# Kernel optimization log

Measured on AMD Instinct MI355X. Metric: run time of the kernel, lower is better.

## Reference

```python
import jax, jax.numpy as jnp
import numpy as np

B, N, C = 4, 4096, 1024
H, M = 16, 64          # num_heads, num_landmarks
DH = C // H
SCALE = H ** (-0.5)    # faithful to source: num_heads**-0.5
LN_EPS = 1e-5


def setup_inputs() -> dict:
    key = jax.random.key(0)
    ks = jax.random.split(key, 8)
    s = 0.02
    return {
        "x": jax.random.normal(ks[0], (B, N, C), jnp.float32),
        "ln_w": jnp.ones((C,), jnp.float32),
        "ln_b": jnp.zeros((C,), jnp.float32),
        "qkv_w": jax.random.normal(ks[1], (3 * C, C), jnp.float32) * s,
        "qkv_b": jax.random.normal(ks[2], (3 * C,), jnp.float32) * s,
        "gamma_w": jax.random.normal(ks[3], (C, C), jnp.float32) * s,
        "gamma_b": jax.random.normal(ks[4], (C,), jnp.float32) * s,
        "proj_w": jax.random.normal(ks[5], (C, C), jnp.float32) * s,
        "proj_b": jax.random.normal(ks[6], (C,), jnp.float32) * s,
    }


def _iterative_inv(K, n_iter=6):
    # Newton-Schulz pseudo-inverse on [..., M, M]
    Id = jnp.eye(K.shape[-1], dtype=K.dtype)
    KA = jnp.abs(K)
    V0 = KA.sum(axis=-2, keepdims=True).max(axis=-1, keepdims=True)
    VI = KA.sum(axis=-1, keepdims=True).max(axis=-2, keepdims=True)
    V = jnp.swapaxes(K, -2, -1) / (V0 * VI)
    for _ in range(n_iter):
        KV = K @ V
        V = 0.25 * V @ (13.0 * Id - KV @ (15.0 * Id - KV @ (7.0 * Id - KV)))
    return V


def reference(x, ln_w, ln_b, qkv_w, qkv_b, gamma_w, gamma_b, proj_w, proj_b):
    # LayerNorm
    mu = x.mean(axis=-1, keepdims=True)
    var = x.var(axis=-1, keepdims=True)
    xn = (x - mu) * jax.lax.rsqrt(var + LN_EPS) * ln_w + ln_b
    # qkv: (B,N,3C) -> (3,B,H,N,DH)
    qkv = (xn @ qkv_w.T + qkv_b).reshape(B, N, 3, H, DH).transpose(2, 0, 3, 1, 4)
    q, k, v = qkv[0], qkv[1], qkv[2]
    # landmarks: mean-pool segments of length N//M, then scale
    q_lm = q.reshape(B, H, M, N // M, DH).mean(axis=-2) * SCALE  # (B,H,M,DH)
    k_lm = k.reshape(B, H, M, N // M, DH).mean(axis=-2) * SCALE
    attn1 = jax.nn.softmax(jnp.einsum('bhnd,bhmd->bhnm', q, k_lm), axis=-1)    # (B,H,N,M)
    attn2 = jax.nn.softmax(jnp.einsum('bhmd,bhld->bhml', q_lm, k_lm), axis=-1)  # (B,H,M,M)
    attn3 = jax.nn.softmax(jnp.einsum('bhmd,bhnd->bhmn', q_lm, k), axis=-1)    # (B,H,M,N)
    attn2_inv = _iterative_inv(attn2)
    out = attn1 @ (attn2_inv @ (attn3 @ v))            # (B,H,N,DH)
    out = out.transpose(0, 2, 1, 3).reshape(B, N, C)
    out = out @ gamma_w.T + gamma_b                    # LipNorm=True branch
    out = out @ proj_w.T + proj_b                      # proj (dropout p=0 is identity)
    return out
```

## Files before the change

kernel.cpp:

```cpp
#include <hip/hip_runtime.h>
#include <stdint.h>

typedef unsigned short u16;
typedef short bf16x8 __attribute__((ext_vector_type(8)));
typedef float f32x4 __attribute__((ext_vector_type(4)));

#define MFMA16(a, b, c) __builtin_amdgcn_mfma_f32_16x16x32_bf16((a), (b), (c), 0, 0, 0)

static __device__ __forceinline__ float bfu2f(u16 u) {
  union { unsigned int i; float f; } z; z.i = ((unsigned int)u) << 16; return z.f;
}
static __device__ __forceinline__ u16 f2bfu(float f) {
  union { float f; unsigned int i; } z; z.f = f;
  unsigned int i = z.i;
  return (u16)((i + 0x7fffu + ((i >> 16) & 1u)) >> 16);
}

__device__ __forceinline__ void gload_lds16(const void* g, void* l) {
  __builtin_amdgcn_global_load_lds((const __attribute__((address_space(1))) void*)g,
                                   (__attribute__((address_space(3))) void*)l, 16, 0, 0);
}

__global__ __launch_bounds__(256) void ln_kernel(
    const float* __restrict__ x, const float* __restrict__ w,
    const float* __restrict__ b, u16* __restrict__ xn) {
  int row = blockIdx.x;
  int t = threadIdx.x;
  const float4* xr = (const float4*)(x + (size_t)row * 1024);
  float4 v = xr[t];
  float s = v.x + v.y + v.z + v.w;
  float ss = v.x * v.x + v.y * v.y + v.z * v.z + v.w * v.w;
#pragma unroll
  for (int m = 1; m < 64; m <<= 1) { s += __shfl_xor(s, m); ss += __shfl_xor(ss, m); }
  __shared__ float sb[4], ssb[4];
  int lane = t & 63, wvi = t >> 6;
  if (lane == 0) { sb[wvi] = s; ssb[wvi] = ss; }
  __syncthreads();
  s = sb[0] + sb[1] + sb[2] + sb[3];
  ss = ssb[0] + ssb[1] + ssb[2] + ssb[3];
  float mu = s * (1.0f / 1024.0f);
  float var = ss * (1.0f / 1024.0f) - mu * mu;
  float rstd = rsqrtf(var + 1e-5f);
  float4 wv4 = ((const float4*)w)[t];
  float4 bv4 = ((const float4*)b)[t];
  ushort4 o;
  o.x = f2bfu((v.x - mu) * rstd * wv4.x + bv4.x);
  o.y = f2bfu((v.y - mu) * rstd * wv4.y + bv4.y);
  o.z = f2bfu((v.z - mu) * rstd * wv4.z + bv4.z);
  o.w = f2bfu((v.w - mu) * rstd * wv4.w + bv4.w);
  ((ushort4*)xn)[(size_t)row * 256 + t] = o;
}

__global__ void cvt3_kernel(const float* __restrict__ a, u16* __restrict__ oa, int na,
                            const float* __restrict__ b, u16* __restrict__ ob, int nb,
                            const float* __restrict__ c, u16* __restrict__ oc, int nc) {
  int total = (na + nb + nc) >> 2;
  for (int i = blockIdx.x * blockDim.x + threadIdx.x; i < total; i += gridDim.x * blockDim.x) {
    int j = i << 2;
    const float* s; u16* d; int off;
    if (j < na) { s = a; d = oa; off = j; }
    else if (j < na + nb) { s = b; d = ob; off = j - na; }
    else { s = c; d = oc; off = j - na - nb; }
    float4 v = *(const float4*)(s + off);
    ushort4 o;
    o.x = f2bfu(v.x); o.y = f2bfu(v.y); o.z = f2bfu(v.z); o.w = f2bfu(v.w);
    *(ushort4*)(d + off) = o;
  }
}

template <int MODE>
__global__ __launch_bounds__(512, 2) void gemm_bt(
    const u16* __restrict__ A, const u16* __restrict__ Bw,
    const float* __restrict__ bias,
    float* __restrict__ Cf, u16* __restrict__ Cb,
    u16* __restrict__ Qo, u16* __restrict__ Ko, u16* __restrict__ Vo,
    int M, int N, int K) {
  __shared__ __attribute__((aligned(16))) u16 As[2][16384];
  __shared__ __attribute__((aligned(16))) u16 Bs[2][16384];
  int tid = threadIdx.x;
  int lane = tid & 63;
  int w = tid >> 6;
  int wr = w >> 2, wc = w & 3;
  int r16 = lane & 15, hi = lane >> 4;
  int l8 = lane >> 3, li = lane & 7;
  int bx = blockIdx.x, by = blockIdx.y;

  const char* Abase = (const char*)(A + (size_t)by * 256 * K);
  const char* Bbase = (const char*)(Bw + (size_t)bx * 256 * K);
  size_t rowbytes = (size_t)K * 2;
  int colsw = (li ^ l8) << 4;
  int nkt = K >> 6;

  f32x4 z4 = {0.f, 0.f, 0.f, 0.f};
  f32x4 acc[8][4];
#pragma unroll
  for (int m = 0; m < 8; ++m)
#pragma unroll
    for (int n = 0; n < 4; ++n) acc[m][n] = z4;

#define SG_A(buf, t, r0)                                                      \
  gload_lds16(Abase + (size_t)((r0) + w * 8 + l8) * rowbytes + ((t) << 7) +   \
                  colsw,                                                      \
              (char*)As[buf] + ((r0) + w * 8) * 128)
#define SG_B(buf, t, r0)                                                      \
  gload_lds16(Bbase + (size_t)((r0) + w * 8 + l8) * rowbytes + ((t) << 7) +   \
                  colsw,                                                      \
              (char*)Bs[buf] + ((r0) + w * 8) * 128)

  SG_A(0, 0, 0); SG_A(0, 0, 64); SG_A(0, 0, 128); SG_A(0, 0, 192);
  SG_B(0, 0, 0); SG_B(0, 0, 64); SG_B(0, 0, 128); SG_B(0, 0, 192);
  SG_A(1, 1, 0); SG_A(1, 1, 128); SG_B(1, 1, 0); SG_B(1, 1, 64);
  SG_A(1, 1, 64); SG_A(1, 1, 192);
  asm volatile("s_waitcnt vmcnt(6)" ::: "memory");
  __builtin_amdgcn_s_barrier();
  __builtin_amdgcn_sched_barrier(0);

  int buf = 0;
  bf16x8 af[4][2], bfr[4][2];

#define LDA(mh)                                                               \
  _Pragma("unroll") for (int m = 0; m < 4; ++m) {                             \
    int row = wr * 128 + (mh) * 64 + m * 16 + r16;                            \
    int sw = (row & 7) << 4;                                                  \
    _Pragma("unroll") for (int kk = 0; kk < 2; ++kk)                          \
        af[m][kk] = *(const bf16x8*)(ab + row * 128 +                         \
                                     (((kk << 6) | (hi << 4)) ^ sw));         \
  }
#define LDB(nh)                                                               \
  _Pragma("unroll") for (int n = 0; n < 2; ++n) {                             \
    int row = wc * 64 + (nh) * 32 + n * 16 + r16;                             \
    int sw = (row & 7) << 4;                                                  \
    _Pragma("unroll") for (int kk = 0; kk < 2; ++kk)                          \
        bfr[(nh) * 2 + n][kk] = *(const bf16x8*)(ab2 + row * 128 +            \
                                     (((kk << 6) | (hi << 4)) ^ sw));         \
  }
#define MM(mh, nh)                                                            \
  __builtin_amdgcn_s_setprio(1);                                              \
  _Pragma("unroll") for (int kk = 0; kk < 2; ++kk)                            \
      _Pragma("unroll") for (int m = 0; m < 4; ++m)                           \
          _Pragma("unroll") for (int n = 0; n < 2; ++n)                       \
              acc[(mh) * 4 + m][(nh) * 2 + n] =                               \
      MFMA16(af[m][kk], bfr[(nh) * 2 + n][kk], acc[(mh) * 4 + m][(nh) * 2 + n]); \
  __builtin_amdgcn_s_setprio(0)

#define BAR1                                                                  \
  __builtin_amdgcn_s_barrier();                                               \
  __builtin_amdgcn_sched_barrier(0)
#define BAR2                                                                  \
  __builtin_amdgcn_sched_barrier(0);                                          \
  __builtin_amdgcn_s_barrier();                                               \
  __builtin_amdgcn_sched_barrier(0)

  for (int t = 0; t < nkt; ++t) {
    const char* ab = (const char*)As[buf];
    const char* ab2 = (const char*)Bs[buf];
    bool s1 = (t + 1 < nkt), s2 = (t + 2 < nkt);
    LDA(0);
    LDB(0);
    if (s1) { SG_B(buf ^ 1, t + 1, 128); SG_B(buf ^ 1, t + 1, 192); }
    BAR1;
    MM(0, 0);
    BAR2;
    LDB(1);
    if (s2) { SG_A(buf, t + 2, 0); SG_A(buf, t + 2, 128); }
    BAR1;
    MM(0, 1);
    BAR2;
    LDA(1);
    if (s2) { SG_B(buf, t + 2, 0); SG_B(buf, t + 2, 64); }
    BAR1;
    MM(1, 0);
    BAR2;
    if (s2) { SG_A(buf, t + 2, 64); SG_A(buf, t + 2, 192); }
    BAR1;
    MM(1, 1);
    __builtin_amdgcn_sched_barrier(0);
    if (s2) {
      asm volatile("s_waitcnt vmcnt(6)" ::: "memory");
    } else {
      asm volatile("s_waitcnt vmcnt(0)" ::: "memory");
    }
    __builtin_amdgcn_s_barrier();
    __builtin_amdgcn_sched_barrier(0);
    buf ^= 1;
  }
#undef SG_A
#undef SG_B
#undef LDA
#undef LDB
#undef MM
#undef BAR1
#undef BAR2

#pragma unroll
  for (int m = 0; m < 8; ++m)
#pragma unroll
    for (int n = 0; n < 4; ++n)
#pragma unroll
      for (int r = 0; r < 4; ++r) {
        int row = by * 256 + wr * 128 + m * 16 + hi * 4 + r;
        int col = bx * 256 + wc * 64 + n * 16 + r16;
        float val = acc[m][n][r] + bias[col];
        if (MODE == 0) {
          Cb[(size_t)row * N + col] = f2bfu(val);
        } else if (MODE == 1) {
          Cf[(size_t)row * N + col] = val;
        } else {
          int bb = row >> 12, nt = row & 4095;
          int jt = col >> 10, h = (col >> 6) & 15, dh = col & 63;
          u16* dst = (jt == 0) ? Qo : (jt == 1) ? Ko : Vo;
          dst[(((size_t)bb * 16 + h) * 4096 + nt) * 64 + dh] = f2bfu(val);
        }
      }
}

__global__ __launch_bounds__(64) void landmark_kernel(
    const u16* __restrict__ Q, const u16* __restrict__ K,
    float* __restrict__ qlmf, u16* __restrict__ qlmb,
    float* __restrict__ klmf, u16* __restrict__ klmb) {
  int bm = blockIdx.x;
  int bh = bm >> 6, m = bm & 63;
  int d = threadIdx.x;
  const u16* src = blockIdx.y ? K : Q;
  const u16* p = src + (((size_t)bh * 4096) + m * 64) * 64 + d;
  float s = 0.f;
#pragma unroll 8
  for (int r = 0; r < 64; ++r) s += bfu2f(p[(size_t)r * 64]);
  float val = s * (0.25f / 64.0f);
  size_t o = (size_t)bh * 4096 + m * 64 + d;
  if (blockIdx.y) { klmf[o] = val; klmb[o] = f2bfu(val); }
  else            { qlmf[o] = val; qlmb[o] = f2bfu(val); }
}

__global__ __launch_bounds__(256) void attn3_pv_kernel(
    const u16* __restrict__ qlmb, const u16* __restrict__ Kmat,
    const u16* __restrict__ Vmat, float* __restrict__ Upart,
    float* __restrict__ rspart) {
  __shared__ __attribute__((aligned(16))) u16 Elds[4][8192];
  int chunk = blockIdx.x, bh = blockIdx.y;
  int tid = threadIdx.x, lane = tid & 63, w = tid >> 6;
  int r16 = lane & 15, hi = lane >> 4;
  int keybase = chunk * 512 + w * 128;
  const u16* kb = Kmat + ((size_t)bh * 4096 + keybase) * 64;
  const u16* vb = Vmat + ((size_t)bh * 4096 + keybase) * 64;
  const u16* qb = qlmb + (size_t)bh * 4096;
  u16* eb = &Elds[w][0];
  f32x4 z4 = {0.f, 0.f, 0.f, 0.f};

  bf16x8 afr[4][2];
#pragma unroll
  for (int m = 0; m < 4; ++m)
#pragma unroll
    for (int kk = 0; kk < 2; ++kk)
      afr[m][kk] = *(const bf16x8*)(qb + (m * 16 + r16) * 64 + kk * 32 + hi * 8);

  float rs[4][4] = {};
  for (int cf = 0; cf < 8; ++cf) {
    f32x4 S[4] = {z4, z4, z4, z4};
#pragma unroll
    for (int kk = 0; kk < 2; ++kk) {
      bf16x8 bfr = *(const bf16x8*)(kb + (size_t)(cf * 16 + r16) * 64 + kk * 32 + hi * 8);
#pragma unroll
      for (int m = 0; m < 4; ++m) S[m] = MFMA16(afr[m][kk], bfr, S[m]);
    }
#pragma unroll
    for (int m = 0; m < 4; ++m)
#pragma unroll
      for (int r = 0; r < 4; ++r) {
        float e = __expf(S[m][r]);
        rs[m][r] += e;
        int row = m * 16 + hi * 4 + r;
        int key = cf * 16 + r16;
        *(u16*)((char*)eb + row * 256 + ((key * 2) ^ ((row & 7) << 4))) = f2bfu(e);
      }
  }
#pragma unroll
  for (int m = 0; m < 4; ++m)
#pragma unroll
    for (int r = 0; r < 4; ++r) {
      float v = rs[m][r];
      v += __shfl_xor(v, 1); v += __shfl_xor(v, 2);
      v += __shfl_xor(v, 4); v += __shfl_xor(v, 8);
      rs[m][r] = v;
    }
  if (r16 == 0) {
    float* rp = rspart + (((size_t)bh * 8 + chunk) * 4 + w) * 64;
#pragma unroll
    for (int m = 0; m < 4; ++m)
#pragma unroll
      for (int r = 0; r < 4; ++r) rp[m * 16 + hi * 4 + r] = rs[m][r];
  }
  __syncthreads();

  f32x4 U[4][4];
#pragma unroll
  for (int m = 0; m < 4; ++m)
#pragma unroll
    for (int df = 0; df < 4; ++df) U[m][df] = z4;
  for (int ks = 0; ks < 4; ++ks) {
    bf16x8 ea[4];
#pragma unroll
    for (int m = 0; m < 4; ++m) {
      int row = m * 16 + r16;
      ea[m] = *(const bf16x8*)((char*)eb + row * 256 + (((ks * 32 + hi * 8) * 2) ^ ((row & 7) << 4)));
    }
#pragma unroll
    for (int df = 0; df < 4; ++df) {
      bf16x8 vb8;
      const u16* vp = vb + (size_t)(ks * 32 + hi * 8) * 64 + df * 16 + r16;
#pragma unroll
      for (int j = 0; j < 8; ++j) ((short*)&vb8)[j] = (short)vp[(size_t)j * 64];
#pragma unroll
      for (int m = 0; m < 4; ++m) U[m][df] = MFMA16(ea[m], vb8, U[m][df]);
    }
  }
  float* up = Upart + (((size_t)bh * 8 + chunk) * 4 + w) * 4096;
#pragma unroll
  for (int m = 0; m < 4; ++m)
#pragma unroll
    for (int df = 0; df < 4; ++df)
#pragma unroll
      for (int r = 0; r < 4; ++r)
        up[(m * 16 + hi * 4 + r) * 64 + df * 16 + r16] = U[m][df][r];
}

__device__ __forceinline__ void mm64(const float (*AT)[68], const float (*Bm)[68],
                                     float (*C)[68], float (*CT)[68],
                                     float alpha, int tid) {
  int tr = (tid >> 4) << 2;
  int tc = (tid & 15) << 2;
  float acc[4][4] = {};
  for (int k = 0; k < 64; ++k) {
    float4 av = *(const float4*)&AT[k][tr];
    float4 bv = *(const float4*)&Bm[k][tc];
    float aa[4] = {av.x, av.y, av.z, av.w};
    float bb[4] = {bv.x, bv.y, bv.z, bv.w};
#pragma unroll
    for (int i = 0; i < 4; ++i)
#pragma unroll
      for (int j = 0; j < 4; ++j) acc[i][j] = fmaf(aa[i], bb[j], acc[i][j]);
  }
#pragma unroll
  for (int i = 0; i < 4; ++i)
#pragma unroll
    for (int j = 0; j < 4; ++j) {
      float vv = acc[i][j] * alpha;
      C[tr + i][tc + j] = vv;
      if (CT) CT[tc + j][tr + i] = vv;
    }
}

__global__ __launch_bounds__(256) void combine_ns_kernel(
    const float* __restrict__ Upart, const float* __restrict__ rspart,
    const float* __restrict__ qlmf, const float* __restrict__ klmf,
    u16* __restrict__ WT) {
  __shared__ __attribute__((aligned(16))) float A2T[64][68];
  __shared__ __attribute__((aligned(16))) float Vv[64][68];
  __shared__ __attribute__((aligned(16))) float VT[64][68];
  __shared__ __attribute__((aligned(16))) float KV[64][68];
  __shared__ __attribute__((aligned(16))) float KVT[64][68];
  __shared__ __attribute__((aligned(16))) float T2[64][68];
  __shared__ __attribute__((aligned(16))) float T4[64][68];
  __shared__ __attribute__((aligned(16))) float Tm[64][68];
  __shared__ float rsum[64], redbuf[64];
  __shared__ float v0s, scal;
  int bh = blockIdx.x, tid = threadIdx.x;

  if (tid < 64) {
    float s = 0.f;
    const float* rp = rspart + (size_t)bh * 32 * 64 + tid;
    for (int p = 0; p < 32; ++p) s += rp[p * 64];
    rsum[tid] = s;
  }
  __syncthreads();
  for (int idx = tid; idx < 4096; idx += 256) {
    float s = 0.f;
    const float* up = Upart + (size_t)bh * 32 * 4096 + idx;
    for (int p = 0; p < 32; ++p) s += up[(size_t)p * 4096];
    int r = idx >> 6, c = idx & 63;
    Tm[r][c] = s / rsum[r];
  }
  for (int idx = tid; idx < 4096; idx += 256) {
    int r = idx >> 6, c = idx & 63;
    Vv[c][r] = qlmf[(size_t)bh * 4096 + idx];
    VT[c][r] = klmf[(size_t)bh * 4096 + idx];
  }
  __syncthreads();
  mm64(&Vv[0], &VT[0], &T2[0], nullptr, 1.0f, tid);
  __syncthreads();
  if (tid < 64) {
    float mx = -1e30f;
    for (int c2 = 0; c2 < 64; ++c2) mx = fmaxf(mx, T2[tid][c2]);
    float s = 0.f;
    for (int c2 = 0; c2 < 64; ++c2) { float e = __expf(T2[tid][c2] - mx); T2[tid][c2] = e; s += e; }
    float inv = 1.f / s;
    for (int c2 = 0; c2 < 64; ++c2) { float p = T2[tid][c2] * inv; T2[tid][c2] = p; A2T[c2][tid] = p; }
  }
  __syncthreads();
  if (tid < 64) {
    float cs = 0.f;
    for (int r2 = 0; r2 < 64; ++r2) cs += fabsf(T2[r2][tid]);
    redbuf[tid] = cs;
  }
  __syncthreads();
  if (tid == 0) {
    float v0 = 0.f;
    for (int c2 = 0; c2 < 64; ++c2) v0 = fmaxf(v0, redbuf[c2]);
    v0s = v0;
  }
  __syncthreads();
  if (tid < 64) {
    float rs2 = 0.f;
    for (int c2 = 0; c2 < 64; ++c2) rs2 += fabsf(T2[tid][c2]);
    redbuf[tid] = rs2;
  }
  __syncthreads();
  if (tid == 0) {
    float vi = 0.f;
    for (int r2 = 0; r2 < 64; ++r2) vi = fmaxf(vi, redbuf[r2]);
    scal = 1.0f / (v0s * vi);
  }
  __syncthreads();
  for (int idx = tid; idx < 4096; idx += 256) {
    int r = idx >> 6, c = idx & 63;
    Vv[r][c] = A2T[r][c] * scal;
    VT[r][c] = T2[r][c] * scal;
  }
  __syncthreads();
  for (int it = 0; it < 6; ++it) {
    mm64(&A2T[0], &Vv[0], &KV[0], &KVT[0], 1.0f, tid);
    __syncthreads();
    for (int idx = tid; idx < 4096; idx += 256) {
      int r = idx >> 6, c = idx & 63;
      T2[r][c] = ((r == c) ? 7.0f : 0.0f) - KV[r][c];
    }
    __syncthreads();
    mm64(&KVT[0], &T2[0], &T4[0], nullptr, 1.0f, tid);
    __syncthreads();
    for (int idx = tid; idx < 4096; idx += 256) {
      int r = idx >> 6, c = idx & 63;
      T2[r][c] = ((r == c) ? 15.0f : 0.0f) - T4[r][c];
    }
    __syncthreads();
    mm64(&KVT[0], &T2[0], &T4[0], nullptr, 1.0f, tid);
    __syncthreads();
    for (int idx = tid; idx < 4096; idx += 256) {
      int r = idx >> 6, c = idx & 63;
      T2[r][c] = ((r == c) ? 13.0f : 0.0f) - T4[r][c];
    }
    __syncthreads();
    mm64(&VT[0], &T2[0], &T4[0], nullptr, 0.25f, tid);
    __syncthreads();
    for (int idx = tid; idx < 4096; idx += 256) {
      int r = idx >> 6, c = idx & 63;
      float vvv = T4[r][c];
      Vv[r][c] = vvv; VT[c][r] = vvv;
    }
    __syncthreads();
  }
  mm64(&VT[0], &Tm[0], &T2[0], nullptr, 1.0f, tid);
  __syncthreads();
  for (int idx = tid; idx < 4096; idx += 256) {
    int r = idx >> 6, c = idx & 63;
    WT[(size_t)bh * 4096 + c * 64 + r] = f2bfu(T2[r][c]);
  }
}

__global__ __launch_bounds__(256) void attn1_out_kernel(
    const u16* __restrict__ Q, const u16* __restrict__ klmb,
    const u16* __restrict__ WT, u16* __restrict__ AO) {
  __shared__ __attribute__((aligned(16))) u16 Elds[4][2048];
  int bh = blockIdx.y;
  int b = bh >> 4, h = bh & 15;
  int tid = threadIdx.x, lane = tid & 63, w = tid >> 6;
  int r16 = lane & 15, hi = lane >> 4;
  int rowbase = blockIdx.x * 128 + w * 32;
  const u16* qb = Q + ((size_t)bh * 4096 + rowbase) * 64;
  const u16* kb = klmb + (size_t)bh * 4096;
  const u16* wtb = WT + (size_t)bh * 4096;
  u16* eb = &Elds[w][0];
  f32x4 z4 = {0.f, 0.f, 0.f, 0.f};

  bf16x8 afr[2][2];
#pragma unroll
  for (int mi = 0; mi < 2; ++mi)
#pragma unroll
    for (int kk = 0; kk < 2; ++kk)
      afr[mi][kk] = *(const bf16x8*)(qb + (mi * 16 + r16) * 64 + kk * 32 + hi * 8);

  float rs[2][4] = {};
  for (int cf = 0; cf < 4; ++cf) {
    f32x4 S[2] = {z4, z4};
#pragma unroll
    for (int kk = 0; kk < 2; ++kk) {
      bf16x8 bfr = *(const bf16x8*)(kb + (cf * 16 + r16) * 64 + kk * 32 + hi * 8);
#pragma unroll
      for (int mi = 0; mi < 2; ++mi) S[mi] = MFMA16(afr[mi][kk], bfr, S[mi]);
    }
#pragma unroll
    for (int mi = 0; mi < 2; ++mi)
#pragma unroll
      for (int r = 0; r < 4; ++r) {
        float e = __expf(S[mi][r]);
        rs[mi][r] += e;
        int row = mi * 16 + hi * 4 + r;
        int key = cf * 16 + r16;
        *(u16*)((char*)eb + row * 128 + ((key * 2) ^ ((row & 7) << 4))) = f2bfu(e);
      }
  }
#pragma unroll
  for (int mi = 0; mi < 2; ++mi)
#pragma unroll
    for (int r = 0; r < 4; ++r) {
      float v = rs[mi][r];
      v += __shfl_xor(v, 1); v += __shfl_xor(v, 2);
      v += __shfl_xor(v, 4); v += __shfl_xor(v, 8);
      rs[mi][r] = v;
    }
  __syncthreads();

  f32x4 O[2][4];
#pragma unroll
  for (int mi = 0; mi < 2; ++mi)
#pragma unroll
    for (int df = 0; df < 4; ++df) O[mi][df] = z4;
  for (int ks = 0; ks < 2; ++ks) {
    bf16x8 ea[2];
#pragma unroll
    for (int mi = 0; mi < 2; ++mi) {
      int row = mi * 16 + r16;
      ea[mi] = *(const bf16x8*)((char*)eb + row * 128 + (((ks * 32 + hi * 8) * 2) ^ ((row & 7) << 4)));
    }
#pragma unroll
    for (int df = 0; df < 4; ++df) {
      bf16x8 wfr = *(const bf16x8*)(wtb + (df * 16 + r16) * 64 + ks * 32 + hi * 8);
#pragma unroll
      for (int mi = 0; mi < 2; ++mi) O[mi][df] = MFMA16(ea[mi], wfr, O[mi][df]);
    }
  }
#pragma unroll
  for (int mi = 0; mi < 2; ++mi)
#pragma unroll
    for (int df = 0; df < 4; ++df)
#pragma unroll
      for (int r = 0; r < 4; ++r) {
        int row = mi * 16 + hi * 4 + r;
        int n = rowbase + row;
        int col = h * 64 + df * 16 + r16;
        float val = O[mi][df][r] / rs[mi][r];
        AO[((size_t)b * 4096 + n) * 1024 + col] = f2bfu(val);
      }
}

extern "C" void kernel_launch(void* const* d_in, const int* in_sizes, int n_in,
                              void* d_out, int out_size, void* d_ws, size_t ws_size,
                              hipStream_t stream) {
  (void)in_sizes; (void)n_in; (void)out_size; (void)ws_size;
  const float* x       = (const float*)d_in[0];
  const float* ln_w    = (const float*)d_in[1];
  const float* ln_b    = (const float*)d_in[2];
  const float* qkv_w   = (const float*)d_in[3];
  const float* qkv_b   = (const float*)d_in[4];
  const float* gamma_w = (const float*)d_in[5];
  const float* gamma_b = (const float*)d_in[6];
  const float* proj_w  = (const float*)d_in[7];
  const float* proj_b  = (const float*)d_in[8];

  char* ws = (char*)d_ws;
  u16* XN     = (u16*)(ws + 0);
  u16* Qb     = (u16*)(ws + 33554432);
  u16* Kb     = (u16*)(ws + 67108864);
  u16* Vb     = (u16*)(ws + 100663296);
  u16* QKVW   = (u16*)(ws + 134217728);
  u16* GW     = (u16*)(ws + 140509184);
  u16* PW     = (u16*)(ws + 142606336);
  float* QLMF = (float*)(ws + 144703488);
  float* KLMF = (float*)(ws + 145752064);
  u16* QLMB   = (u16*)(ws + 146800640);
  u16* KLMB   = (u16*)(ws + 147324928);
  float* RSP  = (float*)(ws + 147849216);
  u16* WTb    = (u16*)(ws + 148373504);
  float* UP   = (float*)XN;

  ln_kernel<<<16384, 256, 0, stream>>>(x, ln_w, ln_b, XN);
  cvt3_kernel<<<2048, 256, 0, stream>>>(qkv_w, QKVW, 3145728,
                                        gamma_w, GW, 1048576,
                                        proj_w, PW, 1048576);
  gemm_bt<2><<<dim3(12, 64), 512, 0, stream>>>(XN, QKVW, qkv_b, nullptr, nullptr,
                                               Qb, Kb, Vb, 16384, 3072, 1024);
  landmark_kernel<<<dim3(4096, 2), 64, 0, stream>>>(Qb, Kb, QLMF, QLMB, KLMF, KLMB);
  attn3_pv_kernel<<<dim3(8, 64), 256, 0, stream>>>(QLMB, Kb, Vb, UP, RSP);
  combine_ns_kernel<<<64, 256, 0, stream>>>(UP, RSP, QLMF, KLMF, WTb);
  attn1_out_kernel<<<dim3(32, 64), 256, 0, stream>>>(Qb, KLMB, WTb, XN);
  gemm_bt<0><<<dim3(4, 64), 512, 0, stream>>>(XN, GW, gamma_b, nullptr, Kb,
                                              nullptr, nullptr, nullptr, 16384, 1024, 1024);
  gemm_bt<1><<<dim3(4, 64), 512, 0, stream>>>(Kb, PW, proj_b, (float*)d_out, nullptr,
                                              nullptr, nullptr, nullptr, 16384, 1024, 1024);
}
```

Before: 378.8 us.

## Store V transposed, swizzle GEMM blocks across XCDs, widen combine kernel

The QKV GEMM epilogue now writes V in a transposed [bh][dh][n] layout using 4-wide vector stores. This lets attn3_pv load each MFMA B fragment as one contiguous 16-byte read instead of eight strided scalar loads. The GEMM block index is remapped so consecutive workgroups are spread across the XCDs, which should improve L2 reuse. The Newton-Schulz combine kernel moves to 512 threads, with each thread computing a 2x4 tile in mm64, to add parallelism to its serial matmul chain. The risks are uncoalesced transposed V writes in the GEMM epilogue and more synchronisation cost per barrier in the combine kernel.

```diff
diff --git a/kernel.cpp b/kernel.cpp
--- a/kernel.cpp
+++ b/kernel.cpp
@@ -83,7 +83,12 @@
   int wr = w >> 2, wc = w & 3;
   int r16 = lane & 15, hi = lane >> 4;
   int l8 = lane >> 3, li = lane & 7;
-  int bx = blockIdx.x, by = blockIdx.y;
+
+  int nwg = gridDim.x * gridDim.y;
+  int flat = blockIdx.y * gridDim.x + blockIdx.x;
+  int q8 = nwg >> 3;
+  int swz = (flat & 7) * q8 + (flat >> 3);
+  int bx = swz % gridDim.x, by = swz / gridDim.x;
 
   const char* Abase = (const char*)(A + (size_t)by * 256 * K);
   const char* Bbase = (const char*)(Bw + (size_t)bx * 256 * K);
@@ -195,23 +200,39 @@
 #pragma unroll
   for (int m = 0; m < 8; ++m)
 #pragma unroll
-    for (int n = 0; n < 4; ++n)
-#pragma unroll
-      for (int r = 0; r < 4; ++r) {
-        int row = by * 256 + wr * 128 + m * 16 + hi * 4 + r;
-        int col = bx * 256 + wc * 64 + n * 16 + r16;
-        float val = acc[m][n][r] + bias[col];
-        if (MODE == 0) {
-          Cb[(size_t)row * N + col] = f2bfu(val);
-        } else if (MODE == 1) {
-          Cf[(size_t)row * N + col] = val;
+    for (int n = 0; n < 4; ++n) {
+      int row0 = by * 256 + wr * 128 + m * 16 + hi * 4;
+      int col = bx * 256 + wc * 64 + n * 16 + r16;
+      if (MODE == 2) {
+        int jt = col >> 10;
+        int h = (col >> 6) & 15, dh = col & 63;
+        int bb = row0 >> 12, nt0 = row0 & 4095;
+        float bcol = bias[col];
+        if (jt == 2) {
+          ushort4 o;
+          o.x = f2bfu(acc[m][n][0] + bcol);
+          o.y = f2bfu(acc[m][n][1] + bcol);
+          o.z = f2bfu(acc[m][n][2] + bcol);
+          o.w = f2bfu(acc[m][n][3] + bcol);
+          *(ushort4*)&Vo[(((size_t)bb * 16 + h) * 64 + dh) * 4096 + nt0] = o;
         } else {
-          int bb = row >> 12, nt = row & 4095;
-          int jt = col >> 10, h = (col >> 6) & 15, dh = col & 63;
-          u16* dst = (jt == 0) ? Qo : (jt == 1) ? Ko : Vo;
-          dst[(((size_t)bb * 16 + h) * 4096 + nt) * 64 + dh] = f2bfu(val);
+          u16* dst = (jt == 0) ? Qo : Ko;
+#pragma unroll
+          for (int r = 0; r < 4; ++r)
+            dst[(((size_t)bb * 16 + h) * 4096 + nt0 + r) * 64 + dh] =
+                f2bfu(acc[m][n][r] + bcol);
+        }
+      } else {
+        float bcol = bias[col];
+#pragma unroll
+        for (int r = 0; r < 4; ++r) {
+          int row = row0 + r;
+          float val = acc[m][n][r] + bcol;
+          if (MODE == 0) Cb[(size_t)row * N + col] = f2bfu(val);
+          else           Cf[(size_t)row * N + col] = val;
         }
       }
+    }
 }
 
 __global__ __launch_bounds__(64) void landmark_kernel(
@@ -234,7 +255,7 @@
 
 __global__ __launch_bounds__(256) void attn3_pv_kernel(
     const u16* __restrict__ qlmb, const u16* __restrict__ Kmat,
-    const u16* __restrict__ Vmat, float* __restrict__ Upart,
+    const u16* __restrict__ Vt, float* __restrict__ Upart,
     float* __restrict__ rspart) {
   __shared__ __attribute__((aligned(16))) u16 Elds[4][8192];
   int chunk = blockIdx.x, bh = blockIdx.y;
@@ -242,7 +263,7 @@
   int r16 = lane & 15, hi = lane >> 4;
   int keybase = chunk * 512 + w * 128;
   const u16* kb = Kmat + ((size_t)bh * 4096 + keybase) * 64;
-  const u16* vb = Vmat + ((size_t)bh * 4096 + keybase) * 64;
+  const u16* vtb = Vt + (size_t)bh * 262144;
   const u16* qb = qlmb + (size_t)bh * 4096;
   u16* eb = &Elds[w][0];
   f32x4 z4 = {0.f, 0.f, 0.f, 0.f};
@@ -306,10 +327,8 @@
     }
 #pragma unroll
     for (int df = 0; df < 4; ++df) {
-      bf16x8 vb8;
-      const u16* vp = vb + (size_t)(ks * 32 + hi * 8) * 64 + df * 16 + r16;
-#pragma unroll
-      for (int j = 0; j < 8; ++j) ((short*)&vb8)[j] = (short)vp[(size_t)j * 64];
+      bf16x8 vb8 = *(const bf16x8*)(vtb + (size_t)(df * 16 + r16) * 4096 +
+                                    keybase + ks * 32 + hi * 8);
 #pragma unroll
       for (int m = 0; m < 4; ++m) U[m][df] = MFMA16(ea[m], vb8, U[m][df]);
     }
@@ -327,21 +346,21 @@
 __device__ __forceinline__ void mm64(const float (*AT)[68], const float (*Bm)[68],
                                      float (*C)[68], float (*CT)[68],
                                      float alpha, int tid) {
-  int tr = (tid >> 4) << 2;
+  int tr = (tid >> 4) << 1;
   int tc = (tid & 15) << 2;
-  float acc[4][4] = {};
+  float acc[2][4] = {};
   for (int k = 0; k < 64; ++k) {
-    float4 av = *(const float4*)&AT[k][tr];
+    float2 av = *(const float2*)&AT[k][tr];
     float4 bv = *(const float4*)&Bm[k][tc];
-    float aa[4] = {av.x, av.y, av.z, av.w};
+    float aa[2] = {av.x, av.y};
     float bb[4] = {bv.x, bv.y, bv.z, bv.w};
 #pragma unroll
-    for (int i = 0; i < 4; ++i)
+    for (int i = 0; i < 2; ++i)
 #pragma unroll
       for (int j = 0; j < 4; ++j) acc[i][j] = fmaf(aa[i], bb[j], acc[i][j]);
   }
 #pragma unroll
-  for (int i = 0; i < 4; ++i)
+  for (int i = 0; i < 2; ++i)
 #pragma unroll
     for (int j = 0; j < 4; ++j) {
       float vv = acc[i][j] * alpha;
@@ -350,7 +369,7 @@
     }
 }
 
-__global__ __launch_bounds__(256) void combine_ns_kernel(
+__global__ __launch_bounds__(512) void combine_ns_kernel(
     const float* __restrict__ Upart, const float* __restrict__ rspart,
     const float* __restrict__ qlmf, const float* __restrict__ klmf,
     u16* __restrict__ WT) {
@@ -373,14 +392,14 @@
     rsum[tid] = s;
   }
   __syncthreads();
-  for (int idx = tid; idx < 4096; idx += 256) {
+  for (int idx = tid; idx < 4096; idx += 512) {
     float s = 0.f;
     const float* up = Upart + (size_t)bh * 32 * 4096 + idx;
     for (int p = 0; p < 32; ++p) s += up[(size_t)p * 4096];
     int r = idx >> 6, c = idx & 63;
     Tm[r][c] = s / rsum[r];
   }
-  for (int idx = tid; idx < 4096; idx += 256) {
+  for (int idx = tid; idx < 4096; idx += 512) {
     int r = idx >> 6, c = idx & 63;
     Vv[c][r] = qlmf[(size_t)bh * 4096 + idx];
     VT[c][r] = klmf[(size_t)bh * 4096 + idx];
@@ -421,7 +440,7 @@
     scal = 1.0f / (v0s * vi);
   }
   __syncthreads();
-  for (int idx = tid; idx < 4096; idx += 256) {
+  for (int idx = tid; idx < 4096; idx += 512) {
     int r = idx >> 6, c = idx & 63;
     Vv[r][c] = A2T[r][c] * scal;
     VT[r][c] = T2[r][c] * scal;
@@ -430,28 +449,28 @@
   for (int it = 0; it < 6; ++it) {
     mm64(&A2T[0], &Vv[0], &KV[0], &KVT[0], 1.0f, tid);
     __syncthreads();
-    for (int idx = tid; idx < 4096; idx += 256) {
+    for (int idx = tid; idx < 4096; idx += 512) {
       int r = idx >> 6, c = idx & 63;
       T2[r][c] = ((r == c) ? 7.0f : 0.0f) - KV[r][c];
     }
     __syncthreads();
     mm64(&KVT[0], &T2[0], &T4[0], nullptr, 1.0f, tid);
     __syncthreads();
-    for (int idx = tid; idx < 4096; idx += 256) {
+    for (int idx = tid; idx < 4096; idx += 512) {
       int r = idx >> 6, c = idx & 63;
       T2[r][c] = ((r == c) ? 15.0f : 0.0f) - T4[r][c];
     }
     __syncthreads();
     mm64(&KVT[0], &T2[0], &T4[0], nullptr, 1.0f, tid);
     __syncthreads();
-    for (int idx = tid; idx < 4096; idx += 256) {
+    for (int idx = tid; idx < 4096; idx += 512) {
       int r = idx >> 6, c = idx & 63;
       T2[r][c] = ((r == c) ? 13.0f : 0.0f) - T4[r][c];
     }
     __syncthreads();
     mm64(&VT[0], &T2[0], &T4[0], nullptr, 0.25f, tid);
     __syncthreads();
-    for (int idx = tid; idx < 4096; idx += 256) {
+    for (int idx = tid; idx < 4096; idx += 512) {
       int r = idx >> 6, c = idx & 63;
       float vvv = T4[r][c];
       Vv[r][c] = vvv; VT[c][r] = vvv;
@@ -460,7 +479,7 @@
   }
   mm64(&VT[0], &Tm[0], &T2[0], nullptr, 1.0f, tid);
   __syncthreads();
-  for (int idx = tid; idx < 4096; idx += 256) {
+  for (int idx = tid; idx < 4096; idx += 512) {
     int r = idx >> 6, c = idx & 63;
     WT[(size_t)bh * 4096 + c * 64 + r] = f2bfu(T2[r][c]);
   }
@@ -590,7 +609,7 @@
                                                Qb, Kb, Vb, 16384, 3072, 1024);
   landmark_kernel<<<dim3(4096, 2), 64, 0, stream>>>(Qb, Kb, QLMF, QLMB, KLMF, KLMB);
   attn3_pv_kernel<<<dim3(8, 64), 256, 0, stream>>>(QLMB, Kb, Vb, UP, RSP);
-  combine_ns_kernel<<<64, 256, 0, stream>>>(UP, RSP, QLMF, KLMF, WTb);
+  combine_ns_kernel<<<64, 512, 0, stream>>>(UP, RSP, QLMF, KLMF, WTb);
   attn1_out_kernel<<<dim3(32, 64), 256, 0, stream>>>(Qb, KLMB, WTb, XN);
   gemm_bt<0><<<dim3(4, 64), 512, 0, stream>>>(XN, GW, gamma_b, nullptr, Kb,
                                               nullptr, nullptr, nullptr, 16384, 1024, 1024);
```

After: 579.1 us. 52.9% more time.
